# Kernel optimization log

Measured on AMD Instinct MI355X. Metric: run time of the kernel, lower is better.

Reference implementation:

```python
import jax, jax.numpy as jnp
import numpy as np

N_NODES = 131072
N_EDGES = 2097152
N_FEAT = 128
N_GRAPHS = 2048
EPS = 1e-5
LEAKY_SLOPE = 0.01


def setup_inputs() -> dict:
    key = jax.random.key(0)
    ks = jax.random.split(key, 8)
    x = jax.random.normal(ks[0], (N_NODES, N_FEAT), dtype=jnp.float32)
    edge_index = jax.random.randint(ks[1], (2, N_EDGES), 0, N_NODES, dtype=jnp.int32)
    batch = jnp.sort(jax.random.randint(ks[2], (N_NODES,), 0, N_GRAPHS, dtype=jnp.int32))
    # Glorot-ish init for weights
    W1 = jax.random.normal(ks[3], (N_FEAT, 64), dtype=jnp.float32) / np.sqrt(N_FEAT)
    W2 = jax.random.normal(ks[4], (64, 128), dtype=jnp.float32) / np.sqrt(64)
    Wo = jax.random.normal(ks[5], (128, 1), dtype=jnp.float32) / np.sqrt(128)
    return {
        'x': x, 'edge_index': edge_index, 'batch': batch,
        'W1': W1, 'b1': jnp.zeros((64,), jnp.float32),
        'gamma1': jnp.ones((64,), jnp.float32), 'beta1': jnp.zeros((64,), jnp.float32),
        'W2': W2, 'b2': jnp.zeros((128,), jnp.float32),
        'gamma2': jnp.ones((128,), jnp.float32), 'beta2': jnp.zeros((128,), jnp.float32),
        'Wo': Wo, 'bo': jnp.zeros((1,), jnp.float32),
    }


def _gcn_conv(x, W, b, src, dst, norm, num_nodes):
    # PyG GCNConv: transform, then sym-normalized aggregation over edges (incl. self loops)
    xw = x @ W                                   # [N, C_out]
    msg = xw[src] * norm[:, None]                # gather + scale  [E+N, C_out]
    agg = jax.ops.segment_sum(msg, dst, num_segments=num_nodes)
    return agg + b


def _batchnorm(x, gamma, beta):
    # training-mode BatchNorm1d: batch stats over node dim, biased variance
    mu = jnp.mean(x, axis=0)
    var = jnp.mean(jnp.square(x - mu), axis=0)
    return gamma * (x - mu) * jax.lax.rsqrt(var + EPS) + beta


def reference(x, edge_index, batch, W1, b1, gamma1, beta1, W2, b2, gamma2, beta2, Wo, bo):
    num_nodes = x.shape[0]
    loop = jnp.arange(num_nodes, dtype=edge_index.dtype)
    src = jnp.concatenate([edge_index[0], loop])
    dst = jnp.concatenate([edge_index[1], loop])
    # symmetric normalization: deg over (A + I), norm = d^-1/2[src] * d^-1/2[dst]
    deg = jax.ops.segment_sum(jnp.ones_like(src, dtype=x.dtype), dst, num_segments=num_nodes)
    dinv = jax.lax.rsqrt(deg)  # deg >= 1 due to self loops
    norm = dinv[src] * dinv[dst]

    h = _gcn_conv(x, W1, b1, src, dst, norm, num_nodes)
    h = jax.nn.leaky_relu(_batchnorm(h, gamma1, beta1), LEAKY_SLOPE)
    h = _gcn_conv(h, W2, b2, src, dst, norm, num_nodes)
    h = jax.nn.leaky_relu(_batchnorm(h, gamma2, beta2), LEAKY_SLOPE)

    # global_mean_pool over graph ids
    sums = jax.ops.segment_sum(h, batch, num_segments=N_GRAPHS)
    cnts = jax.ops.segment_sum(jnp.ones((num_nodes,), h.dtype), batch, num_segments=N_GRAPHS)
    pooled = sums / jnp.maximum(cnts, 1.0)[:, None]
    return pooled @ Wo + bo
```

## Files before the change

### kernel.cpp

```cpp
#include <hip/hip_runtime.h>
#include <hip/hip_fp16.h>

#define NN 131072
#define NE 2097152
#define NT (NE + NN)
#define NTP (NE + 16 * NN)
#define NG 2048
#define NB 256
#define NPB 512
#define CH 256
#define ECH (NE / CH)
#define EPSV 1e-5f

typedef __fp16 half4v __attribute__((ext_vector_type(4)));
typedef float float4v __attribute__((ext_vector_type(4)));

__global__ void k_scan1(const int* __restrict__ in, int* __restrict__ out,
                        int* __restrict__ bsums, int n) {
    __shared__ int tmp[1024];
    int t = threadIdx.x;
    int gid = blockIdx.x * 1024 + t;
    int v = (gid < n) ? in[gid] : 0;
    tmp[t] = v;
    __syncthreads();
    for (int off = 1; off < 1024; off <<= 1) {
        int add = (t >= off) ? tmp[t - off] : 0;
        __syncthreads();
        tmp[t] += add;
        __syncthreads();
    }
    if (gid < n) out[gid] = tmp[t] - v;
    if (t == 1023) bsums[blockIdx.x] = tmp[t];
}
__global__ void k_scan_add(int* __restrict__ out, const int* __restrict__ bs, int n) {
    int gid = blockIdx.x * 1024 + threadIdx.x;
    if (gid < n) out[gid] += bs[blockIdx.x];
}

__global__ __launch_bounds__(256) void k_chist(const int* __restrict__ dst, int* __restrict__ ghist_t,
                                               float* __restrict__ statsZ,
                                               __half* __restrict__ sentA, __half* __restrict__ sentB) {
    __shared__ int h[NB];
    int c = blockIdx.x, tid = threadIdx.x;
    if (c == 0) {
        statsZ[tid] = 0.f; statsZ[tid + 256] = 0.f;
        statsZ[tid + 512] = 0.f; statsZ[tid + 768] = 0.f;
        if (tid < 64) {
            sentA[tid] = __float2half(0.f);
            sentB[tid] = __float2half(0.f);
        }
    }
    h[tid] = 0;
    __syncthreads();
    const int* d = dst + (long)c * ECH;
    for (int i = tid; i < ECH; i += 256) atomicAdd(&h[d[i] >> 9], 1);
    __syncthreads();
    ghist_t[tid * CH + c] = h[tid];
}
__global__ __launch_bounds__(256) void k_cscatter(const int* __restrict__ src, const int* __restrict__ dst,
                                                  const int* __restrict__ scanned, int* __restrict__ packed) {
    __shared__ int cur[NB];
    int c = blockIdx.x, tid = threadIdx.x;
    cur[tid] = scanned[tid * CH + c];
    __syncthreads();
    const int* s = src + (long)c * ECH;
    const int* d = dst + (long)c * ECH;
    for (int i = tid; i < ECH; i += 256) {
        int dv = d[i], sv = s[i];
        int p = atomicAdd(&cur[dv >> 9], 1);
        packed[p] = sv | ((dv & 511) << 17);
    }
}
__global__ __launch_bounds__(512) void k_fine(const int* __restrict__ packed,
                                              const int* __restrict__ scanned,
                                              int2* __restrict__ ninfo, float* __restrict__ dinv,
                                              int* __restrict__ srcs) {
    __shared__ int hist[NPB], sc[NPB], cursor[NPB];
    int b = blockIdx.x, tid = threadIdx.x;
    int ebeg = scanned[b * CH];
    int eend = (b == NB - 1) ? NE : scanned[(b + 1) * CH];
    hist[tid] = 0;
    __syncthreads();
    for (int e = ebeg + tid; e < eend; e += NPB)
        atomicAdd(&hist[packed[e] >> 17], 1);
    __syncthreads();
    int cnt = hist[tid] + 1;
    int pc = (cnt + 15) & ~15;
    sc[tid] = pc;
    __syncthreads();
    for (int off = 1; off < NPB; off <<= 1) {
        int v = (tid >= off) ? sc[tid - off] : 0;
        __syncthreads();
        sc[tid] += v;
        __syncthreads();
    }
    int rbase = ebeg + b * 8192;
    int base = rbase + sc[tid] - pc;
    int n = (b << 9) | tid;
    ninfo[n] = make_int2(base, pc);
    dinv[n] = rsqrtf((float)cnt);
    srcs[base] = n;
    cursor[tid] = base + 1;
    __syncthreads();
    for (int e = ebeg + tid; e < eend; e += NPB) {
        int p = packed[e];
        int pos = atomicAdd(&cursor[p >> 17], 1);
        srcs[pos] = p & 131071;
    }
    __syncthreads();
    for (int q = base + cnt; q < base + pc; ++q) srcs[q] = NN;
}

__global__ __launch_bounds__(256) void k_gemm1(const float* __restrict__ A,
                                               const float* __restrict__ W,
                                               const float* __restrict__ dinv,
                                               __half* __restrict__ out) {
    __shared__ __fp16 as_[64 * 132];
    __shared__ __fp16 ws_[64 * 132];
    int tid = threadIdx.x;
    long row0 = (long)blockIdx.x * 64;
    const float4v* Ag = (const float4v*)(A + row0 * 128);
#pragma unroll
    for (int i = 0; i < 8; ++i) {
        int flat = tid + i * 256;
        int row = flat >> 5, k4 = flat & 31;
        float4v v = Ag[flat];
        half4v h = {(__fp16)v.x, (__fp16)v.y, (__fp16)v.z, (__fp16)v.w};
        *(half4v*)&as_[row * 132 + k4 * 4] = h;
    }
#pragma unroll
    for (int i = 0; i < 32; ++i) {
        int flat = tid + i * 256;
        int k = flat >> 6, n = flat & 63;
        ws_[n * 132 + k] = (__fp16)W[flat];
    }
    __syncthreads();
    int w = tid >> 6, l = tid & 63;
    int lr = l & 15, lg = l >> 4;
    float4v acc[4] = {};
    for (int k0 = 0; k0 < 128; k0 += 16) {
        half4v a = *(const half4v*)&as_[(w * 16 + lr) * 132 + k0 + lg * 4];
#pragma unroll
        for (int t4 = 0; t4 < 4; ++t4) {
            half4v b = *(const half4v*)&ws_[(t4 * 16 + lr) * 132 + k0 + lg * 4];
            acc[t4] = __builtin_amdgcn_mfma_f32_16x16x16f16(a, b, acc[t4], 0, 0, 0);
        }
    }
    float dv[4];
#pragma unroll
    for (int r = 0; r < 4; ++r) dv[r] = dinv[row0 + w * 16 + lg * 4 + r];
#pragma unroll
    for (int t4 = 0; t4 < 4; ++t4)
#pragma unroll
        for (int r = 0; r < 4; ++r) {
            long row = row0 + w * 16 + lg * 4 + r;
            out[row * 64 + t4 * 16 + lr] = __float2half(acc[t4][r] * dv[r]);
        }
}

__global__ __launch_bounds__(256) void k_gemm2(const __half* __restrict__ A,
                                               const float* __restrict__ W,
                                               __half* __restrict__ out,
                                               float* __restrict__ pS, float* __restrict__ pQ) {
    __shared__ __fp16 as_[64 * 68];
    __shared__ __fp16 ws_[128 * 68];
    __shared__ float redS[16][128], redQ[16][128];
    int tid = threadIdx.x;
    long row0 = (long)blockIdx.x * 64;
    const int4* Ag = (const int4*)(A + row0 * 64);
#pragma unroll
    for (int i = 0; i < 2; ++i) {
        int flat8 = tid + i * 256;
        int row = flat8 >> 3, h8 = flat8 & 7;
        int4 v = Ag[flat8];
        *(half4v*)&as_[row * 68 + h8 * 8]     = *(half4v*)&v;
        *(half4v*)&as_[row * 68 + h8 * 8 + 4] = *((half4v*)&v + 1);
    }
#pragma unroll
    for (int i = 0; i < 32; ++i) {
        int flat = tid + i * 256;
        int k = flat >> 7, n = flat & 127;
        ws_[n * 68 + k] = (__fp16)W[flat];
    }
    __syncthreads();
    int w = tid >> 6, l = tid & 63;
    int lr = l & 15, lg = l >> 4;
    float4v acc[8] = {};
    for (int k0 = 0; k0 < 64; k0 += 16) {
        half4v a = *(const half4v*)&as_[(w * 16 + lr) * 68 + k0 + lg * 4];
#pragma unroll
        for (int t4 = 0; t4 < 8; ++t4) {
            half4v b = *(const half4v*)&ws_[(t4 * 16 + lr) * 68 + k0 + lg * 4];
            acc[t4] = __builtin_amdgcn_mfma_f32_16x16x16f16(a, b, acc[t4], 0, 0, 0);
        }
    }
    int band = w * 4 + lg;
#pragma unroll
    for (int t4 = 0; t4 < 8; ++t4) {
        float cs = acc[t4][0] + acc[t4][1] + acc[t4][2] + acc[t4][3];
        float cq = acc[t4][0] * acc[t4][0] + acc[t4][1] * acc[t4][1] +
                   acc[t4][2] * acc[t4][2] + acc[t4][3] * acc[t4][3];
        redS[band][t4 * 16 + lr] = cs;
        redQ[band][t4 * 16 + lr] = cq;
    }
#pragma unroll
    for (int t4 = 0; t4 < 8; ++t4)
#pragma unroll
        for (int r = 0; r < 4; ++r) {
            long row = row0 + w * 16 + lg * 4 + r;
            out[row * 128 + t4 * 16 + lr] = __float2half(acc[t4][r]);
        }
    __syncthreads();
    if (tid < 128) {
        float s = 0.f, q = 0.f;
#pragma unroll
        for (int t = 0; t < 16; ++t) { s += redS[t][tid]; q += redQ[t][tid]; }
        pS[blockIdx.x * 128 + tid] = s;
        pQ[blockIdx.x * 128 + tid] = q;
    }
}

__global__ void k_redstats(const float* __restrict__ pS, const float* __restrict__ pQ,
                           float* __restrict__ sums, float* __restrict__ sqs) {
    int c = threadIdx.x;
    int rbeg = blockIdx.x * 32;
    float a = 0.f;
    if (c < 128) {
        for (int r = 0; r < 32; ++r) a += pS[(rbeg + r) * 128 + c];
        atomicAdd(&sums[c], a);
    } else {
        int cc = c - 128;
        for (int r = 0; r < 32; ++r) a += pQ[(rbeg + r) * 128 + cc];
        atomicAdd(&sqs[cc], a);
    }
}

__global__ __launch_bounds__(256) void k_agg(const __half2* __restrict__ feat2,
                                             const int2* __restrict__ ninfo,
                                             const int* __restrict__ srcs,
                                             const float* __restrict__ dinv,
                                             __half2* __restrict__ out) {
    int wid = (blockIdx.x * 256 + threadIdx.x) >> 6;
    int lane = threadIdx.x & 63;
    int hi = lane >> 5;
    int c = lane & 31;
    int2 ni = ninfo[wid];
    int e0 = ni.x, pd = ni.y;
    int eend = e0 + pd;
    float ax = 0.f, ay = 0.f;
    int e = e0;
    for (; e + 32 <= eend; e += 32) {
        int i0 = srcs[e + hi * 8 + (c & 7)];
        int i1 = srcs[e + 16 + hi * 8 + (c & 7)];
#pragma unroll
        for (int j = 0; j < 8; ++j) {
            int s = __shfl(i0, j, 32);
            float2 f = __half22float2(feat2[(long)s * 32 + c]);
            ax += f.x;
            ay += f.y;
        }
#pragma unroll
        for (int j = 0; j < 8; ++j) {
            int s = __shfl(i1, j, 32);
            float2 f = __half22float2(feat2[(long)s * 32 + c]);
            ax += f.x;
            ay += f.y;
        }
    }
    if (e < eend) {
        int i0 = srcs[e + hi * 8 + (c & 7)];
#pragma unroll
        for (int j = 0; j < 8; ++j) {
            int s = __shfl(i0, j, 32);
            float2 f = __half22float2(feat2[(long)s * 32 + c]);
            ax += f.x;
            ay += f.y;
        }
    }
    ax += __shfl_xor(ax, 32);
    ay += __shfl_xor(ay, 32);
    if (hi == 0) {
        float dn = dinv[wid];
        out[(long)wid * 32 + c] = __floats2half2_rn(ax * dn, ay * dn);
    }
}

__global__ __launch_bounds__(256) void k_stats64h(const __half2* __restrict__ h2,
                                                  float* __restrict__ sums, float* __restrict__ sqs) {
    __shared__ float sx[256], sy[256], qx[256], qy[256];
    int tid = threadIdx.x;
    int c = tid & 31, rg = tid >> 5;
    long row0 = (long)blockIdx.x * 1024;
    float ax = 0.f, ay = 0.f, bx = 0.f, by = 0.f;
    for (int i = rg; i < 1024; i += 8) {
        float2 f = __half22float2(h2[(row0 + i) * 32 + c]);
        ax += f.x; ay += f.y; bx += f.x * f.x; by += f.y * f.y;
    }
    sx[tid] = ax; sy[tid] = ay; qx[tid] = bx; qy[tid] = by;
    __syncthreads();
    if (tid < 32) {
        float tax = 0.f, tay = 0.f, tbx = 0.f, tby = 0.f;
#pragma unroll
        for (int g = 0; g < 8; ++g) {
            tax += sx[g * 32 + tid]; tay += sy[g * 32 + tid];
            tbx += qx[g * 32 + tid]; tby += qy[g * 32 + tid];
        }
        atomicAdd(&sums[2 * tid], tax); atomicAdd(&sums[2 * tid + 1], tay);
        atomicAdd(&sqs[2 * tid], tbx);  atomicAdd(&sqs[2 * tid + 1], tby);
    }
}

__global__ __launch_bounds__(256) void k_apply1h(const __half* __restrict__ h,
                                                 const float* __restrict__ sums,
                                                 const float* __restrict__ sqs,
                                                 const float* __restrict__ gamma,
                                                 const float* __restrict__ beta,
                                                 const float* __restrict__ dinv,
                                                 __half* __restrict__ out) {
    __shared__ float sc_[64], sh_[64];
    int tid = threadIdx.x;
    if (tid < 64) {
        const float invN = 1.0f / (float)NN;
        float mean = sums[tid] * invN;
        float var = sqs[tid] * invN - mean * mean;
        float inv = rsqrtf(var + EPSV);
        float s = gamma[tid] * inv;
        sc_[tid] = s;
        sh_[tid] = beta[tid] - mean * s;
    }
    __syncthreads();
    long idx = (long)blockIdx.x * 256 + tid;
    int row = (int)(idx >> 3);
    int cb = (int)(idx & 7) * 8;
    float dv = dinv[row];
    int4 v = ((const int4*)h)[idx];
    __half2* hp = (__half2*)&v;
    int4 o;
    __half2* op = (__half2*)&o;
#pragma unroll
    for (int j = 0; j < 4; ++j) {
        float2 f = __half22float2(hp[j]);
        float y0 = fmaf(f.x, sc_[cb + 2 * j], sh_[cb + 2 * j]);
        float y1 = fmaf(f.y, sc_[cb + 2 * j + 1], sh_[cb + 2 * j + 1]);
        y0 = y0 > 0.f ? y0 : 0.01f * y0;
        y1 = y1 > 0.f ? y1 : 0.01f * y1;
        op[j] = __floats2half2_rn(y0 * dv, y1 * dv);
    }
    ((int4*)out)[idx] = o;
}

__global__ __launch_bounds__(256) void k_pool(const __half* __restrict__ h,
                                              const int* __restrict__ batch,
                                              const float* __restrict__ sums,
                                              const float* __restrict__ sqs,
                                              const float* __restrict__ gamma,
                                              const float* __restrict__ beta,
                                              const float* __restrict__ Wo,
                                              const float* __restrict__ bo,
                                              float* __restrict__ out) {
    __shared__ float accx[4][64], accy[4][64];
    __shared__ float sc_[128], sh_[128];
    __shared__ int range[2];
    int g = blockIdx.x;
    int tid = threadIdx.x;
    int wv = tid >> 6, lane = tid & 63;
    if (tid < 128) {
        const float invN = 1.0f / (float)NN;
        float mean = sums[tid] * invN;
        float var = sqs[tid] * invN - mean * mean;
        float inv = rsqrtf(var + EPSV);
        float s = gamma[tid] * inv;
        sc_[tid] = s;
        sh_[tid] = beta[tid] - mean * s;
    }
    if (tid < 2) {
        int target = g + tid;
        int lo = 0, hi = NN;
        while (lo < hi) {
            int mid = (lo + hi) >> 1;
            if (batch[mid] < target) lo = mid + 1; else hi = mid;
        }
        range[tid] = lo;
    }
    __syncthreads();
    int beg = range[0], cnt = range[1] - range[0];
    float sc0 = sc_[2 * lane], sc1 = sc_[2 * lane + 1];
    float sh0 = sh_[2 * lane], sh1 = sh_[2 * lane + 1];
    float a0 = 0.f, a1 = 0.f;
    for (int i = wv; i < cnt; i += 4) {
        __half2 v = ((const __half2*)(h + (long)(beg + i) * 128))[lane];
        float2 f = __half22float2(v);
        float y0 = fmaf(f.x, sc0, sh0); y0 = y0 > 0.f ? y0 : 0.01f * y0;
        float y1 = fmaf(f.y, sc1, sh1); y1 = y1 > 0.f ? y1 : 0.01f * y1;
        a0 += y0; a1 += y1;
    }
    accx[wv][lane] = a0;
    accy[wv][lane] = a1;
    __syncthreads();
    if (wv == 0) {
        a0 = accx[0][lane] + accx[1][lane] + accx[2][lane] + accx[3][lane];
        a1 = accy[0][lane] + accy[1][lane] + accy[2][lane] + accy[3][lane];
        float v = a0 * Wo[2 * lane] + a1 * Wo[2 * lane + 1];
        v /= fmaxf((float)cnt, 1.f);
#pragma unroll
        for (int m = 32; m; m >>= 1) v += __shfl_xor(v, m);
        if (lane == 0) out[g] = v + bo[0];
    }
}

extern "C" void kernel_launch(void* const* d_in, const int* in_sizes, int n_in,
                              void* d_out, int out_size, void* d_ws, size_t ws_size,
                              hipStream_t stream) {
    const float* x    = (const float*)d_in[0];
    const int* ei     = (const int*)d_in[1];
    const int* batch  = (const int*)d_in[2];
    const float* W1   = (const float*)d_in[3];
    const float* g1   = (const float*)d_in[5];
    const float* be1  = (const float*)d_in[6];
    const float* W2   = (const float*)d_in[7];
    const float* g2   = (const float*)d_in[9];
    const float* be2  = (const float*)d_in[10];
    const float* Wo   = (const float*)d_in[11];
    const float* bo   = (const float*)d_in[12];
    float* out = (float*)d_out;

    const int* esrc = ei;
    const int* edst = ei + NE;

    __half* h2h = (__half*)d_ws;
    __half* bufA = h2h + (size_t)NN * 128;
    __half* bufB = bufA + (size_t)(NN + 1) * 64;
    float* dinv = (float*)(bufB + (size_t)(NN + 1) * 64);
    float* stats = dinv + NN;
    float* sums1 = stats,        *sqs1 = stats + 64;
    float* sums2 = stats + 128,  *sqs2 = stats + 256;
    int2* ninfo = (int2*)(stats + 1024);
    int* srcs   = (int*)(ninfo + NN);
    int* bsums  = srcs + NTP;
    int* bsums2 = bsums + 256;
    int* dummy  = bsums2 + 256;
    float* pS   = (float*)(dummy + 8);
    float* pQ   = pS + 2048 * 128;
    int* ghist_t = (int*)bufA;
    int* scanned = ghist_t + NB * CH;
    int* packed  = (int*)h2h;
    __half* sentA = bufA + (size_t)NN * 64;
    __half* sentB = bufB + (size_t)NN * 64;

    k_chist<<<CH, 256, 0, stream>>>(edst, ghist_t, stats, sentA, sentB);
    k_scan1<<<NB * CH / 1024, 1024, 0, stream>>>(ghist_t, scanned, bsums, NB * CH);
    k_scan1<<<1, 1024, 0, stream>>>(bsums, bsums2, dummy, NB * CH / 1024);
    k_scan_add<<<NB * CH / 1024, 1024, 0, stream>>>(scanned, bsums2, NB * CH);
    k_cscatter<<<CH, 256, 0, stream>>>(esrc, edst, scanned, packed);
    k_fine<<<NB, NPB, 0, stream>>>(packed, scanned, ninfo, dinv, srcs);

    k_gemm1<<<NN / 64, 256, 0, stream>>>(x, W1, dinv, bufA);
    k_agg<<<NN / 4, 256, 0, stream>>>((const __half2*)bufA, ninfo, srcs, dinv, (__half2*)bufB);
    k_stats64h<<<NN / 1024, 256, 0, stream>>>((const __half2*)bufB, sums1, sqs1);
    k_apply1h<<<NN * 64 / 8 / 256, 256, 0, stream>>>(bufB, sums1, sqs1, g1, be1, dinv, bufB);

    k_agg<<<NN / 4, 256, 0, stream>>>((const __half2*)bufB, ninfo, srcs, dinv, (__half2*)bufA);
    k_gemm2<<<NN / 64, 256, 0, stream>>>(bufA, W2, h2h, pS, pQ);
    k_redstats<<<64, 256, 0, stream>>>(pS, pQ, sums2, sqs2);

    k_pool<<<NG, 256, 0, stream>>>(h2h, batch, sums2, sqs2, g2, be2, Wo, bo, out);
}
```

Before: 242.3 us.

## Fuse CSR construction kernels into one cooperative kernel with grid syncs

Replaces six separate launches (coarse histogram, three scan kernels, coarse scatter, fine bucket build) with a single cooperative kernel of 256 blocks of 512 threads that uses grid.sync between phases. The goal is to remove launch overhead and inter-kernel gaps in the graph-preprocessing stage. The scan is restructured as a row reduction, a single-block scan of the row sums, then per-row scans. Grid-wide barriers have their own cost, and each phase now runs on only 256 blocks.

```diff
diff --git a/kernel.cpp b/kernel.cpp
--- a/kernel.cpp
+++ b/kernel.cpp
@@ -1,5 +1,8 @@
 #include <hip/hip_runtime.h>
 #include <hip/hip_fp16.h>
+#include <hip/hip_cooperative_groups.h>
+
+namespace cg = cooperative_groups;
 
 #define NN 131072
 #define NE 2097152
@@ -15,100 +18,124 @@
 typedef __fp16 half4v __attribute__((ext_vector_type(4)));
 typedef float float4v __attribute__((ext_vector_type(4)));
 
-__global__ void k_scan1(const int* __restrict__ in, int* __restrict__ out,
-                        int* __restrict__ bsums, int n) {
-    __shared__ int tmp[1024];
-    int t = threadIdx.x;
-    int gid = blockIdx.x * 1024 + t;
-    int v = (gid < n) ? in[gid] : 0;
-    tmp[t] = v;
-    __syncthreads();
-    for (int off = 1; off < 1024; off <<= 1) {
-        int add = (t >= off) ? tmp[t - off] : 0;
-        __syncthreads();
-        tmp[t] += add;
-        __syncthreads();
-    }
-    if (gid < n) out[gid] = tmp[t] - v;
-    if (t == 1023) bsums[blockIdx.x] = tmp[t];
-}
-__global__ void k_scan_add(int* __restrict__ out, const int* __restrict__ bs, int n) {
-    int gid = blockIdx.x * 1024 + threadIdx.x;
-    if (gid < n) out[gid] += bs[blockIdx.x];
-}
-
-__global__ __launch_bounds__(256) void k_chist(const int* __restrict__ dst, int* __restrict__ ghist_t,
-                                               float* __restrict__ statsZ,
-                                               __half* __restrict__ sentA, __half* __restrict__ sentB) {
-    __shared__ int h[NB];
-    int c = blockIdx.x, tid = threadIdx.x;
-    if (c == 0) {
-        statsZ[tid] = 0.f; statsZ[tid + 256] = 0.f;
-        statsZ[tid + 512] = 0.f; statsZ[tid + 768] = 0.f;
+__global__ __launch_bounds__(512) void k_csr(const int* __restrict__ esrc, const int* __restrict__ edst,
+                                             int* __restrict__ scanned, int* __restrict__ rowsum,
+                                             int* __restrict__ packed,
+                                             int2* __restrict__ ninfo, float* __restrict__ dinv,
+                                             int* __restrict__ srcs,
+                                             float* __restrict__ statsZ,
+                                             __half* __restrict__ sentA, __half* __restrict__ sentB) {
+    cg::grid_group grid = cg::this_grid();
+    __shared__ int shm[1536];
+    int b = blockIdx.x, tid = threadIdx.x;
+
+    if (b == 0) {
+        statsZ[tid] = 0.f; statsZ[tid + 512] = 0.f;
         if (tid < 64) {
             sentA[tid] = __float2half(0.f);
             sentB[tid] = __float2half(0.f);
         }
     }
-    h[tid] = 0;
-    __syncthreads();
-    const int* d = dst + (long)c * ECH;
-    for (int i = tid; i < ECH; i += 256) atomicAdd(&h[d[i] >> 9], 1);
-    __syncthreads();
-    ghist_t[tid * CH + c] = h[tid];
-}
-__global__ __launch_bounds__(256) void k_cscatter(const int* __restrict__ src, const int* __restrict__ dst,
-                                                  const int* __restrict__ scanned, int* __restrict__ packed) {
-    __shared__ int cur[NB];
-    int c = blockIdx.x, tid = threadIdx.x;
-    cur[tid] = scanned[tid * CH + c];
-    __syncthreads();
-    const int* s = src + (long)c * ECH;
-    const int* d = dst + (long)c * ECH;
-    for (int i = tid; i < ECH; i += 256) {
-        int dv = d[i], sv = s[i];
-        int p = atomicAdd(&cur[dv >> 9], 1);
-        packed[p] = sv | ((dv & 511) << 17);
-    }
-}
-__global__ __launch_bounds__(512) void k_fine(const int* __restrict__ packed,
-                                              const int* __restrict__ scanned,
-                                              int2* __restrict__ ninfo, float* __restrict__ dinv,
-                                              int* __restrict__ srcs) {
-    __shared__ int hist[NPB], sc[NPB], cursor[NPB];
-    int b = blockIdx.x, tid = threadIdx.x;
-    int ebeg = scanned[b * CH];
-    int eend = (b == NB - 1) ? NE : scanned[(b + 1) * CH];
-    hist[tid] = 0;
-    __syncthreads();
-    for (int e = ebeg + tid; e < eend; e += NPB)
-        atomicAdd(&hist[packed[e] >> 17], 1);
-    __syncthreads();
-    int cnt = hist[tid] + 1;
-    int pc = (cnt + 15) & ~15;
-    sc[tid] = pc;
-    __syncthreads();
-    for (int off = 1; off < NPB; off <<= 1) {
-        int v = (tid >= off) ? sc[tid - off] : 0;
-        __syncthreads();
-        sc[tid] += v;
-        __syncthreads();
-    }
-    int rbase = ebeg + b * 8192;
-    int base = rbase + sc[tid] - pc;
-    int n = (b << 9) | tid;
-    ninfo[n] = make_int2(base, pc);
-    dinv[n] = rsqrtf((float)cnt);
-    srcs[base] = n;
-    cursor[tid] = base + 1;
-    __syncthreads();
-    for (int e = ebeg + tid; e < eend; e += NPB) {
-        int p = packed[e];
-        int pos = atomicAdd(&cursor[p >> 17], 1);
-        srcs[pos] = p & 131071;
-    }
-    __syncthreads();
-    for (int q = base + cnt; q < base + pc; ++q) srcs[q] = NN;
+    if (tid < NB) shm[tid] = 0;
+    __syncthreads();
+    {
+        const int* d = edst + (long)b * ECH;
+        for (int i = tid; i < ECH; i += 512) atomicAdd(&shm[d[i] >> 9], 1);
+    }
+    __syncthreads();
+    if (tid < NB) scanned[tid * CH + b] = shm[tid];
+    grid.sync();
+
+    {
+        int v = (tid < CH) ? scanned[b * CH + tid] : 0;
+        if (tid < CH) shm[tid] = v;
+        __syncthreads();
+        for (int off = 128; off > 0; off >>= 1) {
+            if (tid < off) shm[tid] += shm[tid + off];
+            __syncthreads();
+        }
+        if (tid == 0) rowsum[b] = shm[0];
+    }
+    grid.sync();
+
+    if (b == 0) {
+        int rv = (tid < NB) ? rowsum[tid] : 0;
+        if (tid < NB) shm[tid] = rv;
+        __syncthreads();
+        for (int off = 1; off < NB; off <<= 1) {
+            int add = (tid < NB && tid >= off) ? shm[tid - off] : 0;
+            __syncthreads();
+            if (tid < NB) shm[tid] += add;
+            __syncthreads();
+        }
+        if (tid < NB) rowsum[tid] = shm[tid] - rv;
+    }
+    grid.sync();
+
+    {
+        int v = (tid < CH) ? scanned[b * CH + tid] : 0;
+        if (tid < CH) shm[tid] = v;
+        __syncthreads();
+        for (int off = 1; off < CH; off <<= 1) {
+            int add = (tid < CH && tid >= off) ? shm[tid - off] : 0;
+            __syncthreads();
+            if (tid < CH) shm[tid] += add;
+            __syncthreads();
+        }
+        if (tid < CH) scanned[b * CH + tid] = shm[tid] - v + rowsum[b];
+    }
+    grid.sync();
+
+    {
+        if (tid < NB) shm[tid] = scanned[tid * CH + b];
+        __syncthreads();
+        const int* s = esrc + (long)b * ECH;
+        const int* d = edst + (long)b * ECH;
+        for (int i = tid; i < ECH; i += 512) {
+            int dv = d[i], sv = s[i];
+            int p = atomicAdd(&shm[dv >> 9], 1);
+            packed[p] = sv | ((dv & 511) << 17);
+        }
+    }
+    grid.sync();
+
+    {
+        int* hist = shm;
+        int* sc = shm + 512;
+        int* cursor = shm + 1024;
+        int ebeg = scanned[b * CH];
+        int eend = (b == NB - 1) ? NE : scanned[(b + 1) * CH];
+        hist[tid] = 0;
+        __syncthreads();
+        for (int e = ebeg + tid; e < eend; e += NPB)
+            atomicAdd(&hist[packed[e] >> 17], 1);
+        __syncthreads();
+        int cnt = hist[tid] + 1;
+        int pc = (cnt + 15) & ~15;
+        sc[tid] = pc;
+        __syncthreads();
+        for (int off = 1; off < NPB; off <<= 1) {
+            int v = (tid >= off) ? sc[tid - off] : 0;
+            __syncthreads();
+            sc[tid] += v;
+            __syncthreads();
+        }
+        int rbase = ebeg + b * 8192;
+        int base = rbase + sc[tid] - pc;
+        int n = (b << 9) | tid;
+        ninfo[n] = make_int2(base, pc);
+        dinv[n] = rsqrtf((float)cnt);
+        srcs[base] = n;
+        cursor[tid] = base + 1;
+        __syncthreads();
+        for (int e = ebeg + tid; e < eend; e += NPB) {
+            int p = packed[e];
+            int pos = atomicAdd(&cursor[p >> 17], 1);
+            srcs[pos] = p & 131071;
+        }
+        __syncthreads();
+        for (int q = base + cnt; q < base + pc; ++q) srcs[q] = NN;
+    }
 }
 
 __global__ __launch_bounds__(256) void k_gemm1(const float* __restrict__ A,
@@ -436,23 +463,20 @@
     float* sums2 = stats + 128,  *sqs2 = stats + 256;
     int2* ninfo = (int2*)(stats + 1024);
     int* srcs   = (int*)(ninfo + NN);
-    int* bsums  = srcs + NTP;
-    int* bsums2 = bsums + 256;
-    int* dummy  = bsums2 + 256;
-    float* pS   = (float*)(dummy + 8);
+    int* rowsum = srcs + NTP;
+    float* pS   = (float*)(rowsum + 256 + 8);
     float* pQ   = pS + 2048 * 128;
-    int* ghist_t = (int*)bufA;
-    int* scanned = ghist_t + NB * CH;
+    int* scanned = (int*)bufA;
     int* packed  = (int*)h2h;
     __half* sentA = bufA + (size_t)NN * 64;
     __half* sentB = bufB + (size_t)NN * 64;
 
-    k_chist<<<CH, 256, 0, stream>>>(edst, ghist_t, stats, sentA, sentB);
-    k_scan1<<<NB * CH / 1024, 1024, 0, stream>>>(ghist_t, scanned, bsums, NB * CH);
-    k_scan1<<<1, 1024, 0, stream>>>(bsums, bsums2, dummy, NB * CH / 1024);
-    k_scan_add<<<NB * CH / 1024, 1024, 0, stream>>>(scanned, bsums2, NB * CH);
-    k_cscatter<<<CH, 256, 0, stream>>>(esrc, edst, scanned, packed);
-    k_fine<<<NB, NPB, 0, stream>>>(packed, scanned, ninfo, dinv, srcs);
+    {
+        void* args[] = {(void*)&esrc, (void*)&edst, (void*)&scanned, (void*)&rowsum,
+                        (void*)&packed, (void*)&ninfo, (void*)&dinv, (void*)&srcs,
+                        (void*)&stats, (void*)&sentA, (void*)&sentB};
+        hipLaunchCooperativeKernel((const void*)k_csr, dim3(NB), dim3(512), args, 0, stream);
+    }
 
     k_gemm1<<<NN / 64, 256, 0, stream>>>(x, W1, dinv, bufA);
     k_agg<<<NN / 4, 256, 0, stream>>>((const __half2*)bufA, ninfo, srcs, dinv, (__half2*)bufB);
```

After: 387.7 us. 60.0% more time.
